# Performance work log

Hardware: AMD Instinct MI355X
Metric: run time of the kernel (lower is better)

## Reference

```python
import jax, jax.numpy as jnp
import numpy as np

B, N, H, D = 8, 2048, 4, 64  # batch, seq, heads (multi_head_count), head_dim
OUT = 256


def setup_inputs() -> dict:
    key = jax.random.key(0)
    ks = jax.random.split(key, 9)
    s = 0.02
    return {
        "x": jax.random.normal(ks[0], (B, N, H * D), dtype=jnp.float32),
        "Wq": jax.random.normal(ks[1], (H, D, D), dtype=jnp.float32) * s,
        "Wk": jax.random.normal(ks[2], (H, D, D), dtype=jnp.float32) * s,
        "Wv": jax.random.normal(ks[3], (H, D, D), dtype=jnp.float32) * s,
        "bq": jnp.zeros((H, D), dtype=jnp.float32),
        "bk": jnp.zeros((H, D), dtype=jnp.float32),
        "bv": jnp.zeros((H, D), dtype=jnp.float32),
        "Wp": jax.random.normal(ks[4], (H * D, OUT), dtype=jnp.float32) * s,
        "bp": jnp.zeros((OUT,), dtype=jnp.float32),
    }


def reference(x, Wq, Wk, Wv, bq, bk, bv, Wp, bp):
    # x: [b, n, h*d] -> [b, h, n, d]
    b, n, _ = x.shape
    xh = x.reshape(b, n, H, D).transpose(0, 2, 1, 3)
    # per-head Q/K/V with per-head weights (heads selected = [0..H-1], deterministic for num_heads==4)
    q = jnp.einsum("bhnd,hde->bhne", xh, Wq) + bq[None, :, None, :]
    k = jnp.einsum("bhnd,hde->bhne", xh, Wk) + bk[None, :, None, :]
    v = jnp.einsum("bhnd,hde->bhne", xh, Wv) + bv[None, :, None, :]
    scale = 1.0 / jnp.sqrt(jnp.asarray(D, dtype=x.dtype))
    scores = jnp.einsum("bhne,bhme->bhnm", q, k) * scale  # [b,h,n,n]
    attn = jax.nn.softmax(scores, axis=-1)
    o = jnp.einsum("bhnm,bhme->bhne", attn, v)  # [b,h,n,d]
    # concat heads: [b, n, h*d], then final projection
    o = o.transpose(0, 2, 1, 3).reshape(b, n, H * D)
    return o @ Wp + bp
```

## Files before the change

### kernel.cpp

```cpp
#include <hip/hip_runtime.h>

typedef __attribute__((ext_vector_type(4)))  float  f32x4;
typedef __attribute__((ext_vector_type(16))) float  f32x16;
typedef __attribute__((ext_vector_type(8)))  __bf16 bf16x8;
typedef __attribute__((ext_vector_type(2)))  unsigned u32x2;

constexpr int Bv = 8, Nv = 2048, Hv = 4, Dv = 64, OUTv = 256, HD = 256;
constexpr int BH = Bv * Hv;
constexpr size_t PH = (size_t)BH * Nv * Dv;

#if __has_builtin(__builtin_amdgcn_exp2f)
#define EXP2(x) __builtin_amdgcn_exp2f(x)
#else
#define EXP2(x) exp2f(x)
#endif

__device__ __forceinline__ unsigned short f2bf(float f) {
    union { __bf16 h; unsigned short u; } r;
    r.h = (__bf16)f;
    return r.u;
}

__device__ __forceinline__ unsigned pk_bf16(float a, float b) {
    union { __bf16 h[2]; unsigned u; } r;
    r.h[0] = (__bf16)a; r.h[1] = (__bf16)b;
    return r.u;
}

__device__ __forceinline__ uint4 pack8(const float* f) {
    uint4 u;
    u.x = pk_bf16(f[0], f[1]);
    u.y = pk_bf16(f[2], f[3]);
    u.z = pk_bf16(f[4], f[5]);
    u.w = pk_bf16(f[6], f[7]);
    return u;
}

__device__ __forceinline__ void swap32(unsigned a, unsigned b, unsigned& lo, unsigned& hi) {
#if __has_builtin(__builtin_amdgcn_permlane32_swap)
    u32x2 r = __builtin_amdgcn_permlane32_swap(a, b, false, false);
    lo = r.x; hi = r.y;
#else
    const int ishi = (threadIdx.x & 63) >> 5;
    unsigned pa = __shfl_xor(a, 32, 64), pb = __shfl_xor(b, 32, 64);
    lo = ishi ? pb : a;
    hi = ishi ? b : pa;
#endif
}

#define GLOBAL_AS __attribute__((address_space(1)))
#define LDS_AS    __attribute__((address_space(3)))

__global__ __launch_bounds__(256) void wconv_kernel(
    const float* __restrict__ Wq, const float* __restrict__ Wk, const float* __restrict__ Wv,
    const float* __restrict__ Wp,
    unsigned short* __restrict__ Wt3, unsigned short* __restrict__ Wpt)
{
    const int idx = blockIdx.x * 256 + threadIdx.x;
    if (idx < 49152) {
        const int m = idx >> 14, r = idx & 16383;
        const int h = r >> 12, e = (r >> 6) & 63, d = r & 63;
        const float* W = (m == 0) ? Wq : ((m == 1) ? Wk : Wv);
        Wt3[idx] = f2bf(W[(h << 12) + d * 64 + e]);
    } else {
        const int r = idx - 49152;
        const int e = r >> 8, c = r & 255;
        Wpt[r] = f2bf(Wp[c * 256 + e]);
    }
}

__global__ __launch_bounds__(256) void qkv_kernel(
    const float* __restrict__ x,
    const unsigned short* __restrict__ Wt3,
    const float* __restrict__ bq, const float* __restrict__ bk, const float* __restrict__ bv,
    unsigned short* __restrict__ Qb, unsigned short* __restrict__ Kb,
    unsigned short* __restrict__ Vt)
{
    const int h = blockIdx.x & 3;
    const int tt = blockIdx.x >> 2;
    const int tok0 = tt * 64;
    const int t = threadIdx.x, l = t & 63, w = t >> 6;
    const int lg = l >> 4, lc = l & 15;

    __shared__ uint4 Xs[64 * 8];
    __shared__ uint4 Ws[3 * 512];
    __shared__ uint4 Os[64 * 8];

#pragma unroll
    for (int k = 0; k < 6; ++k) {
        const int s = k * 256 + t;
        const int m = s >> 9, sm = s & 511;
        const int e = sm >> 3, cp = sm & 7;
        __builtin_amdgcn_global_load_lds(
            (const GLOBAL_AS unsigned int*)(Wt3 + (m << 14) + (h << 12) + (e << 6) + ((cp ^ (e & 7)) << 3)),
            (LDS_AS unsigned int*)((char*)Ws + (k * 256 + w * 64) * 16),
            16, 0, 0);
    }

    {
        const int r = t >> 2, c4 = t & 3;
        const float* src = x + (size_t)(tok0 + r) * HD + h * Dv + c4 * 16;
        float f[16];
        *(float4*)(f)      = *(const float4*)(src);
        *(float4*)(f + 4)  = *(const float4*)(src + 4);
        *(float4*)(f + 8)  = *(const float4*)(src + 8);
        *(float4*)(f + 12) = *(const float4*)(src + 12);
        Xs[r * 8 + ((c4 * 2)     ^ (r & 7))] = pack8(f);
        Xs[r * 8 + ((c4 * 2 + 1) ^ (r & 7))] = pack8(f + 8);
    }
    asm volatile("s_waitcnt vmcnt(0)" ::: "memory");
    __syncthreads();

    const int ar = w * 16 + lc;
    bf16x8 a[2];
    a[0] = ((const bf16x8*)Xs)[ar * 8 + (lg       ^ (ar & 7))];
    a[1] = ((const bf16x8*)Xs)[ar * 8 + ((4 + lg) ^ (ar & 7))];

    f32x4 acc[3][4];
#pragma unroll
    for (int m = 0; m < 3; ++m)
#pragma unroll
        for (int nt = 0; nt < 4; ++nt) acc[m][nt] = (f32x4){0.f, 0.f, 0.f, 0.f};

#pragma unroll
    for (int kk = 0; kk < 2; ++kk) {
#pragma unroll
        for (int m = 0; m < 3; ++m) {
#pragma unroll
            for (int nt = 0; nt < 4; ++nt) {
                const int br = nt * 16 + lc;
                const bf16x8 b = ((const bf16x8*)Ws)[(m << 9) + br * 8 + ((kk * 4 + lg) ^ (br & 7))];
                acc[m][nt] = __builtin_amdgcn_mfma_f32_16x16x32_bf16(a[kk], b, acc[m][nt], 0, 0, 0);
            }
        }
    }

    const int b_ = tok0 >> 11, n_ = tok0 & (Nv - 1);
    const int bh = b_ * Hv + h;
    unsigned short* Os16 = (unsigned short*)Os;
    const float* biases[3] = {bq + h * Dv, bk + h * Dv, bv + h * Dv};
    const float QSCALE = 0.125f * 1.44269504088896340736f;

#pragma unroll
    for (int m = 0; m < 3; ++m) {
        if (m) __syncthreads();
        if (m < 2) {
#pragma unroll
            for (int nt = 0; nt < 4; ++nt) {
                const int e = nt * 16 + lc;
                const float bias = biases[m][e];
#pragma unroll
                for (int j = 0; j < 4; ++j) {
                    float v = acc[m][nt][j] + bias;
                    if (m == 0) v *= QSCALE;
                    const int row = w * 16 + lg * 4 + j;
                    const int ch = (e >> 3) ^ (row & 7);
                    Os16[row * 64 + ch * 8 + (e & 7)] = f2bf(v);
                }
            }
            __syncthreads();
            const int r = t >> 2, c4 = t & 3;
            unsigned short* dst = (m == 0 ? Qb : Kb) + ((size_t)bh * Nv + n_ + r) * Dv + c4 * 16;
            *(uint4*)dst       = Os[r * 8 + ((c4 * 2)     ^ (r & 7))];
            *(uint4*)(dst + 8) = Os[r * 8 + ((c4 * 2 + 1) ^ (r & 7))];
        } else {
#pragma unroll
            for (int nt = 0; nt < 4; ++nt) {
                const int e = nt * 16 + lc;
                const float bias = biases[2][e];
#pragma unroll
                for (int j = 0; j < 4; ++j) {
                    const int tok = w * 16 + lg * 4 + j;
                    const int ch = (tok >> 3) ^ (e & 7);
                    Os16[e * 64 + ch * 8 + (tok & 7)] = f2bf(acc[2][nt][j] + bias);
                }
            }
            __syncthreads();
            const int e = t >> 2, c4 = t & 3;
            unsigned short* dst = Vt + ((size_t)bh * Dv + e) * Nv + n_ + c4 * 16;
            *(uint4*)dst       = Os[e * 8 + ((c4 * 2)     ^ (e & 7))];
            *(uint4*)(dst + 8) = Os[e * 8 + ((c4 * 2 + 1) ^ (e & 7))];
        }
    }
}

__global__ __launch_bounds__(256, 2) void attn_kernel(
    const unsigned short* __restrict__ Qb, const unsigned short* __restrict__ Kb,
    const unsigned short* __restrict__ Vt, unsigned short* __restrict__ Ob)
{
    const int bh = blockIdx.x & 31;
    const int qt = blockIdx.x >> 5;
    const int t = threadIdx.x, w = t >> 6, l = t & 63;
    const int hi = l >> 5, lc = l & 31;

    __shared__ uint4 Ks[2][128 * 8];
    __shared__ uint4 Vs[2][64 * 16];

    const unsigned short* Kg = Kb + (size_t)bh * Nv * Dv;
    const unsigned short* Vg = Vt + (size_t)bh * Dv * Nv;

    const int q_ = qt * 128 + w * 32 + lc;
    const unsigned short* Qrow = Qb + ((size_t)bh * Nv + q_) * Dv;
    bf16x8 qf[4];
#pragma unroll
    for (int kk = 0; kk < 4; ++kk)
        qf[kk] = *(const bf16x8*)(Qrow + kk * 16 + hi * 8);

    auto stage = [&](int buf, int kt) {
#pragma unroll
        for (int k = 0; k < 4; ++k) {
            const int s = k * 256 + t;
            const int base = k * 256 + w * 64;
            {
                const int r = s >> 3, c = (s & 7) ^ (r & 7);
                __builtin_amdgcn_global_load_lds(
                    (const GLOBAL_AS unsigned int*)(Kg + ((size_t)kt * 128 + r) * Dv + c * 8),
                    (LDS_AS unsigned int*)((char*)&Ks[buf][0] + base * 16),
                    16, 0, 0);
            }
            {
                const int r = s >> 4, c = (s & 15) ^ (r & 15);
                __builtin_amdgcn_global_load_lds(
                    (const GLOBAL_AS unsigned int*)(Vg + (size_t)r * Nv + kt * 128 + c * 8),
                    (LDS_AS unsigned int*)((char*)&Vs[buf][0] + base * 16),
                    16, 0, 0);
            }
        }
    };

    f32x16 o0, o1;
#pragma unroll
    for (int i = 0; i < 16; ++i) { o0[i] = 0.f; o1[i] = 0.f; }
    float m_run = -1e30f, l_part = 0.f;

    stage(0, 0);
    asm volatile("s_waitcnt vmcnt(0)" ::: "memory");
    __syncthreads();

    int cur = 0;
    for (int kt = 0; kt < Nv / 128; ++kt) {
        if (kt < Nv / 128 - 1) stage(cur ^ 1, kt + 1);

        const uint4* KsB = &Ks[cur][0];
        const uint4* VsB = &Vs[cur][0];

        f32x16 s4[4];
#pragma unroll
        for (int nt = 0; nt < 4; ++nt) {
#pragma unroll
            for (int i = 0; i < 16; ++i) s4[nt][i] = 0.f;
        }
        __builtin_amdgcn_s_setprio(1);
#pragma unroll
        for (int kk = 0; kk < 4; ++kk) {
#pragma unroll
            for (int nt = 0; nt < 4; ++nt) {
                const int r = nt * 32 + lc;
                const bf16x8 af = *(const bf16x8*)&KsB[r * 8 + ((kk * 2 + hi) ^ (r & 7))];
                s4[nt] = __builtin_amdgcn_mfma_f32_32x32x16_bf16(af, qf[kk], s4[nt], 0, 0, 0);
            }
        }
        __builtin_amdgcn_s_setprio(0);

        float v16[16];
#pragma unroll
        for (int r = 0; r < 16; ++r)
            v16[r] = fmaxf(fmaxf(s4[0][r], s4[1][r]), fmaxf(s4[2][r], s4[3][r]));
#pragma unroll
        for (int st = 8; st; st >>= 1)
#pragma unroll
            for (int r = 0; r < st; ++r) v16[r] = fmaxf(v16[r], v16[r + st]);
        float tm = fmaxf(v16[0], __shfl_xor(v16[0], 32, 64));

        if (!__all(tm <= m_run + 8.f)) {
            const float m_new = fmaxf(m_run, tm);
            const float sc = EXP2(m_run - m_new);
            m_run = m_new;
            l_part *= sc;
#pragma unroll
            for (int i = 0; i < 16; ++i) { o0[i] *= sc; o1[i] *= sc; }
        }

        float tsa[4] = {0.f, 0.f, 0.f, 0.f};
#pragma unroll
        for (int nt = 0; nt < 4; ++nt) {
#pragma unroll
            for (int r = 0; r < 16; ++r) {
                const float p = EXP2(s4[nt][r] - m_run);
                s4[nt][r] = p;
                tsa[r & 3] += p;
            }
            unsigned c[8];
#pragma unroll
            for (int i = 0; i < 8; ++i) c[i] = pk_bf16(s4[nt][2 * i], s4[nt][2 * i + 1]);

            unsigned d0a, d2a, d1a, d3a, d0b, d2b, d1b, d3b;
            swap32(c[0], c[2], d0a, d2a);
            swap32(c[1], c[3], d1a, d3a);
            swap32(c[4], c[6], d0b, d2b);
            swap32(c[5], c[7], d1b, d3b);

            union { unsigned u[4]; bf16x8 v; } pf0, pf1;
            pf0.u[0] = d0a; pf0.u[1] = d1a; pf0.u[2] = d2a; pf0.u[3] = d3a;
            pf1.u[0] = d0b; pf1.u[1] = d1b; pf1.u[2] = d2b; pf1.u[3] = d3b;

            __builtin_amdgcn_s_setprio(1);
#pragma unroll
            for (int kslow = 0; kslow < 2; ++kslow) {
                const bf16x8 pf = kslow ? pf1.v : pf0.v;
                {
                    const int row = lc;
                    const int ch = (nt * 4 + kslow * 2 + hi) ^ (row & 15);
                    const bf16x8 vf = *(const bf16x8*)&VsB[row * 16 + ch];
                    o0 = __builtin_amdgcn_mfma_f32_32x32x16_bf16(vf, pf, o0, 0, 0, 0);
                }
                {
                    const int row = 32 + lc;
                    const int ch = (nt * 4 + kslow * 2 + hi) ^ (row & 15);
                    const bf16x8 vf = *(const bf16x8*)&VsB[row * 16 + ch];
                    o1 = __builtin_amdgcn_mfma_f32_32x32x16_bf16(vf, pf, o1, 0, 0, 0);
                }
            }
            __builtin_amdgcn_s_setprio(0);
        }
        l_part += (tsa[0] + tsa[1]) + (tsa[2] + tsa[3]);

        if (kt < Nv / 128 - 1) {
            asm volatile("s_waitcnt vmcnt(0)" ::: "memory");
            __syncthreads();
            cur ^= 1;
        }
    }

    const float lf = l_part + __shfl_xor(l_part, 32, 64);
    const float inv = 1.0f / lf;
    const int b_ = bh >> 2, h_ = bh & 3;
    unsigned short* orow = Ob + ((size_t)b_ * Nv + q_) * HD + h_ * Dv;
#pragma unroll
    for (int g = 0; g < 4; ++g) {
        uint2 ua, ub;
        ua.x = pk_bf16(o0[g * 4 + 0] * inv, o0[g * 4 + 1] * inv);
        ua.y = pk_bf16(o0[g * 4 + 2] * inv, o0[g * 4 + 3] * inv);
        ub.x = pk_bf16(o1[g * 4 + 0] * inv, o1[g * 4 + 1] * inv);
        ub.y = pk_bf16(o1[g * 4 + 2] * inv, o1[g * 4 + 3] * inv);
        *(uint2*)(orow + 8 * g + 4 * hi)      = ua;
        *(uint2*)(orow + 32 + 8 * g + 4 * hi) = ub;
    }
}

__global__ __launch_bounds__(256) void proj_kernel(
    const unsigned short* __restrict__ Ob, const unsigned short* __restrict__ Wpt,
    const float* __restrict__ bp, float* __restrict__ out)
{
    const int tok0 = blockIdx.x * 64;
    const int t = threadIdx.x, w = t >> 6, l = t & 63;
    const int hi = l >> 5, lc = l & 31;
    const int tw = w >> 1;

    __shared__ uint4 SH[2560];

    f32x16 acc[4];
#pragma unroll
    for (int ct = 0; ct < 4; ++ct)
#pragma unroll
        for (int i = 0; i < 16; ++i) acc[ct][i] = 0.f;

    for (int kt = 0; kt < 4; ++kt) {
        const int c0 = kt * 64;
        if (kt) __syncthreads();
#pragma unroll
        for (int j = 0; j < 10; ++j) {
            const int s = j * 256 + t;
            const int base = j * 256 + w * 64;
            if (s < 512) {
                const int r = s >> 3, cp = s & 7;
                __builtin_amdgcn_global_load_lds(
                    (const GLOBAL_AS unsigned int*)(Ob + (size_t)(tok0 + r) * HD + c0 + ((cp ^ (r & 7)) << 3)),
                    (LDS_AS unsigned int*)((char*)SH + base * 16),
                    16, 0, 0);
            } else {
                const int sm = s - 512;
                const int e = sm >> 3, cp = sm & 7;
                __builtin_amdgcn_global_load_lds(
                    (const GLOBAL_AS unsigned int*)(Wpt + (size_t)e * HD + c0 + ((cp ^ (e & 7)) << 3)),
                    (LDS_AS unsigned int*)((char*)SH + base * 16),
                    16, 0, 0);
            }
        }
        asm volatile("s_waitcnt vmcnt(0)" ::: "memory");
        __syncthreads();

        const bf16x8* Osh = (const bf16x8*)SH;
        const bf16x8* Wsh = (const bf16x8*)(SH + 512);
        const int r = tw * 32 + lc;
#pragma unroll
        for (int kk = 0; kk < 4; ++kk) {
            const bf16x8 af = Osh[r * 8 + ((kk * 2 + hi) ^ (r & 7))];
#pragma unroll
            for (int ct = 0; ct < 4; ++ct) {
                const int e = (w & 1) * 128 + ct * 32 + lc;
                const bf16x8 bf = Wsh[e * 8 + ((kk * 2 + hi) ^ (e & 7))];
                acc[ct] = __builtin_amdgcn_mfma_f32_32x32x16_bf16(af, bf, acc[ct], 0, 0, 0);
            }
        }
    }

#pragma unroll
    for (int ct = 0; ct < 4; ++ct) {
        const int e = (w & 1) * 128 + ct * 32 + lc;
        const float bias = bp[e];
#pragma unroll
        for (int r = 0; r < 16; ++r) {
            const int tok = tok0 + tw * 32 + (r & 3) + 8 * (r >> 2) + 4 * hi;
            out[(size_t)tok * OUTv + e] = acc[ct][r] + bias;
        }
    }
}

extern "C" void kernel_launch(void* const* d_in, const int* in_sizes, int n_in,
                              void* d_out, int out_size, void* d_ws, size_t ws_size,
                              hipStream_t stream)
{
    const float* x  = (const float*)d_in[0];
    const float* Wq = (const float*)d_in[1];
    const float* Wk = (const float*)d_in[2];
    const float* Wv = (const float*)d_in[3];
    const float* bq = (const float*)d_in[4];
    const float* bk = (const float*)d_in[5];
    const float* bv = (const float*)d_in[6];
    const float* Wp = (const float*)d_in[7];
    const float* bp = (const float*)d_in[8];
    float* out = (float*)d_out;

    unsigned short* us = (unsigned short*)d_ws;
    unsigned short* Qb  = us;
    unsigned short* Kb  = us + PH;
    unsigned short* Vt  = us + 2 * PH;
    unsigned short* Ob  = us + 3 * PH;
    unsigned short* Wt3 = us + 4 * PH;
    unsigned short* Wpt = Wt3 + 49152;

    wconv_kernel<<<448, 256, 0, stream>>>(Wq, Wk, Wv, Wp, Wt3, Wpt);
    qkv_kernel<<<(Bv * Nv / 64) * Hv, 256, 0, stream>>>(x, Wt3, bq, bk, bv, Qb, Kb, Vt);
    attn_kernel<<<(Nv / 128) * BH, 256, 0, stream>>>(Qb, Kb, Vt, Ob);
    proj_kernel<<<Bv * Nv / 64, 256, 0, stream>>>(Ob, Wpt, bp, out);
}
```

Baseline: 154.6 us.

## Pre-convert x to bf16, merge QKV epilogue, double-buffer smaller proj tiles

x is converted to bf16 in the weight-conversion kernel, so the QKV kernel can load it straight into LDS with global_load_lds instead of doing fp32 loads and packing in registers. The QKV epilogue now writes Q, K and V^T into three LDS regions in one pass with two barriers instead of six. The projection kernel moves to 32-token tiles with double-buffered LDS staging, which overlaps loads with MFMA and doubles the grid. The cost is an extra bf16 round trip of x through global memory.

```diff
diff --git a/kernel.cpp b/kernel.cpp
--- a/kernel.cpp
+++ b/kernel.cpp
@@ -52,11 +52,21 @@
 #define LDS_AS    __attribute__((address_space(3)))
 
 __global__ __launch_bounds__(256) void wconv_kernel(
+    const float* __restrict__ x,
     const float* __restrict__ Wq, const float* __restrict__ Wk, const float* __restrict__ Wv,
     const float* __restrict__ Wp,
+    unsigned short* __restrict__ Xb,
     unsigned short* __restrict__ Wt3, unsigned short* __restrict__ Wpt)
 {
-    const int idx = blockIdx.x * 256 + threadIdx.x;
+    if (blockIdx.x < 2048) {
+        const size_t g = ((size_t)blockIdx.x * 256 + threadIdx.x) * 8;
+        float f[8];
+        *(float4*)(f)     = *(const float4*)(x + g);
+        *(float4*)(f + 4) = *(const float4*)(x + g + 4);
+        *(uint4*)(Xb + g) = pack8(f);
+        return;
+    }
+    const int idx = (blockIdx.x - 2048) * 256 + threadIdx.x;
     if (idx < 49152) {
         const int m = idx >> 14, r = idx & 16383;
         const int h = r >> 12, e = (r >> 6) & 63, d = r & 63;
@@ -70,7 +80,7 @@
 }
 
 __global__ __launch_bounds__(256) void qkv_kernel(
-    const float* __restrict__ x,
+    const unsigned short* __restrict__ Xb,
     const unsigned short* __restrict__ Wt3,
     const float* __restrict__ bq, const float* __restrict__ bk, const float* __restrict__ bv,
     unsigned short* __restrict__ Qb, unsigned short* __restrict__ Kb,
@@ -87,6 +97,16 @@
     __shared__ uint4 Os[64 * 8];
 
 #pragma unroll
+    for (int k = 0; k < 2; ++k) {
+        const int slot = k * 256 + t;
+        const int r = slot >> 3, cp = slot & 7;
+        const int c = cp ^ (r & 7);
+        __builtin_amdgcn_global_load_lds(
+            (const GLOBAL_AS unsigned int*)(Xb + (size_t)(tok0 + r) * HD + h * Dv + c * 8),
+            (LDS_AS unsigned int*)((char*)Xs + (k * 256 + w * 64) * 16),
+            16, 0, 0);
+    }
+#pragma unroll
     for (int k = 0; k < 6; ++k) {
         const int s = k * 256 + t;
         const int m = s >> 9, sm = s & 511;
@@ -96,18 +116,6 @@
             (LDS_AS unsigned int*)((char*)Ws + (k * 256 + w * 64) * 16),
             16, 0, 0);
     }
-
-    {
-        const int r = t >> 2, c4 = t & 3;
-        const float* src = x + (size_t)(tok0 + r) * HD + h * Dv + c4 * 16;
-        float f[16];
-        *(float4*)(f)      = *(const float4*)(src);
-        *(float4*)(f + 4)  = *(const float4*)(src + 4);
-        *(float4*)(f + 8)  = *(const float4*)(src + 8);
-        *(float4*)(f + 12) = *(const float4*)(src + 12);
-        Xs[r * 8 + ((c4 * 2)     ^ (r & 7))] = pack8(f);
-        Xs[r * 8 + ((c4 * 2 + 1) ^ (r & 7))] = pack8(f + 8);
-    }
     asm volatile("s_waitcnt vmcnt(0)" ::: "memory");
     __syncthreads();
 
@@ -137,50 +145,42 @@
 
     const int b_ = tok0 >> 11, n_ = tok0 & (Nv - 1);
     const int bh = b_ * Hv + h;
-    unsigned short* Os16 = (unsigned short*)Os;
-    const float* biases[3] = {bq + h * Dv, bk + h * Dv, bv + h * Dv};
     const float QSCALE = 0.125f * 1.44269504088896340736f;
 
-#pragma unroll
-    for (int m = 0; m < 3; ++m) {
-        if (m) __syncthreads();
-        if (m < 2) {
-#pragma unroll
-            for (int nt = 0; nt < 4; ++nt) {
-                const int e = nt * 16 + lc;
-                const float bias = biases[m][e];
-#pragma unroll
-                for (int j = 0; j < 4; ++j) {
-                    float v = acc[m][nt][j] + bias;
-                    if (m == 0) v *= QSCALE;
-                    const int row = w * 16 + lg * 4 + j;
-                    const int ch = (e >> 3) ^ (row & 7);
-                    Os16[row * 64 + ch * 8 + (e & 7)] = f2bf(v);
-                }
-            }
-            __syncthreads();
-            const int r = t >> 2, c4 = t & 3;
-            unsigned short* dst = (m == 0 ? Qb : Kb) + ((size_t)bh * Nv + n_ + r) * Dv + c4 * 16;
-            *(uint4*)dst       = Os[r * 8 + ((c4 * 2)     ^ (r & 7))];
-            *(uint4*)(dst + 8) = Os[r * 8 + ((c4 * 2 + 1) ^ (r & 7))];
-        } else {
-#pragma unroll
-            for (int nt = 0; nt < 4; ++nt) {
-                const int e = nt * 16 + lc;
-                const float bias = biases[2][e];
-#pragma unroll
-                for (int j = 0; j < 4; ++j) {
-                    const int tok = w * 16 + lg * 4 + j;
-                    const int ch = (tok >> 3) ^ (e & 7);
-                    Os16[e * 64 + ch * 8 + (tok & 7)] = f2bf(acc[2][nt][j] + bias);
-                }
-            }
-            __syncthreads();
-            const int e = t >> 2, c4 = t & 3;
-            unsigned short* dst = Vt + ((size_t)bh * Dv + e) * Nv + n_ + c4 * 16;
-            *(uint4*)dst       = Os[e * 8 + ((c4 * 2)     ^ (e & 7))];
-            *(uint4*)(dst + 8) = Os[e * 8 + ((c4 * 2 + 1) ^ (e & 7))];
-        }
+    __syncthreads();
+    {
+        unsigned short* Os16 = (unsigned short*)Os;
+        unsigned short* Ks16 = (unsigned short*)Xs;
+        unsigned short* Vs16 = (unsigned short*)Ws;
+#pragma unroll
+        for (int nt = 0; nt < 4; ++nt) {
+            const int e = nt * 16 + lc;
+            const float bq_ = bq[h * Dv + e];
+            const float bk_ = bk[h * Dv + e];
+            const float bv_ = bv[h * Dv + e];
+#pragma unroll
+            for (int j = 0; j < 4; ++j) {
+                const int row = w * 16 + lg * 4 + j;
+                const int ch = (e >> 3) ^ (row & 7);
+                Os16[row * 64 + ch * 8 + (e & 7)] = f2bf((acc[0][nt][j] + bq_) * QSCALE);
+                Ks16[row * 64 + ch * 8 + (e & 7)] = f2bf(acc[1][nt][j] + bk_);
+                const int chv = (row >> 3) ^ (e & 7);
+                Vs16[e * 64 + chv * 8 + (row & 7)] = f2bf(acc[2][nt][j] + bv_);
+            }
+        }
+    }
+    __syncthreads();
+    {
+        const int r = t >> 2, c4 = t & 3;
+        unsigned short* dq = Qb + ((size_t)bh * Nv + n_ + r) * Dv + c4 * 16;
+        *(uint4*)dq       = Os[r * 8 + ((c4 * 2)     ^ (r & 7))];
+        *(uint4*)(dq + 8) = Os[r * 8 + ((c4 * 2 + 1) ^ (r & 7))];
+        unsigned short* dk = Kb + ((size_t)bh * Nv + n_ + r) * Dv + c4 * 16;
+        *(uint4*)dk       = Xs[r * 8 + ((c4 * 2)     ^ (r & 7))];
+        *(uint4*)(dk + 8) = Xs[r * 8 + ((c4 * 2 + 1) ^ (r & 7))];
+        unsigned short* dv = Vt + ((size_t)bh * Dv + r) * Nv + n_ + c4 * 16;
+        *(uint4*)dv       = Ws[r * 8 + ((c4 * 2)     ^ (r & 7))];
+        *(uint4*)(dv + 8) = Ws[r * 8 + ((c4 * 2 + 1) ^ (r & 7))];
     }
 }
 
@@ -352,66 +352,73 @@
     const unsigned short* __restrict__ Ob, const unsigned short* __restrict__ Wpt,
     const float* __restrict__ bp, float* __restrict__ out)
 {
-    const int tok0 = blockIdx.x * 64;
+    const int tok0 = blockIdx.x * 32;
     const int t = threadIdx.x, w = t >> 6, l = t & 63;
     const int hi = l >> 5, lc = l & 31;
-    const int tw = w >> 1;
-
-    __shared__ uint4 SH[2560];
-
-    f32x16 acc[4];
-#pragma unroll
-    for (int ct = 0; ct < 4; ++ct)
-#pragma unroll
-        for (int i = 0; i < 16; ++i) acc[ct][i] = 0.f;
-
-    for (int kt = 0; kt < 4; ++kt) {
+
+    __shared__ uint4 SH[2][2304];
+
+    auto stage = [&](int buf, int kt) {
         const int c0 = kt * 64;
-        if (kt) __syncthreads();
-#pragma unroll
-        for (int j = 0; j < 10; ++j) {
+#pragma unroll
+        for (int j = 0; j < 9; ++j) {
             const int s = j * 256 + t;
             const int base = j * 256 + w * 64;
-            if (s < 512) {
+            if (s < 256) {
                 const int r = s >> 3, cp = s & 7;
                 __builtin_amdgcn_global_load_lds(
                     (const GLOBAL_AS unsigned int*)(Ob + (size_t)(tok0 + r) * HD + c0 + ((cp ^ (r & 7)) << 3)),
-                    (LDS_AS unsigned int*)((char*)SH + base * 16),
+                    (LDS_AS unsigned int*)((char*)&SH[buf][0] + base * 16),
                     16, 0, 0);
             } else {
-                const int sm = s - 512;
-                const int e = sm >> 3, cp = sm & 7;
+                const int s2 = s - 256;
+                const int e = s2 >> 3, cp = s2 & 7;
                 __builtin_amdgcn_global_load_lds(
                     (const GLOBAL_AS unsigned int*)(Wpt + (size_t)e * HD + c0 + ((cp ^ (e & 7)) << 3)),
-                    (LDS_AS unsigned int*)((char*)SH + base * 16),
+                    (LDS_AS unsigned int*)((char*)&SH[buf][0] + base * 16),
                     16, 0, 0);
             }
         }
-        asm volatile("s_waitcnt vmcnt(0)" ::: "memory");
+    };
+
+    f32x16 acc[2];
+#pragma unroll
+    for (int ct = 0; ct < 2; ++ct)
+#pragma unroll
+        for (int i = 0; i < 16; ++i) acc[ct][i] = 0.f;
+
+    stage(0, 0);
+    for (int kt = 0; kt < 4; ++kt) {
+        if (kt < 3) {
+            stage((kt + 1) & 1, kt + 1);
+            asm volatile("s_waitcnt vmcnt(9)" ::: "memory");
+        } else {
+            asm volatile("s_waitcnt vmcnt(0)" ::: "memory");
+        }
         __syncthreads();
 
-        const bf16x8* Osh = (const bf16x8*)SH;
-        const bf16x8* Wsh = (const bf16x8*)(SH + 512);
-        const int r = tw * 32 + lc;
+        const bf16x8* Osh = (const bf16x8*)&SH[kt & 1][0];
+        const bf16x8* Wsh = (const bf16x8*)&SH[kt & 1][256];
 #pragma unroll
         for (int kk = 0; kk < 4; ++kk) {
-            const bf16x8 af = Osh[r * 8 + ((kk * 2 + hi) ^ (r & 7))];
-#pragma unroll
-            for (int ct = 0; ct < 4; ++ct) {
-                const int e = (w & 1) * 128 + ct * 32 + lc;
-                const bf16x8 bf = Wsh[e * 8 + ((kk * 2 + hi) ^ (e & 7))];
-                acc[ct] = __builtin_amdgcn_mfma_f32_32x32x16_bf16(af, bf, acc[ct], 0, 0, 0);
-            }
-        }
-    }
-
-#pragma unroll
-    for (int ct = 0; ct < 4; ++ct) {
-        const int e = (w & 1) * 128 + ct * 32 + lc;
+            const bf16x8 af = Osh[lc * 8 + ((kk * 2 + hi) ^ (lc & 7))];
+#pragma unroll
+            for (int ct = 0; ct < 2; ++ct) {
+                const int e = w * 64 + ct * 32 + lc;
+                const bf16x8 bf_ = Wsh[e * 8 + ((kk * 2 + hi) ^ (e & 7))];
+                acc[ct] = __builtin_amdgcn_mfma_f32_32x32x16_bf16(af, bf_, acc[ct], 0, 0, 0);
+            }
+        }
+        __syncthreads();
+    }
+
+#pragma unroll
+    for (int ct = 0; ct < 2; ++ct) {
+        const int e = w * 64 + ct * 32 + lc;
         const float bias = bp[e];
 #pragma unroll
         for (int r = 0; r < 16; ++r) {
-            const int tok = tok0 + tw * 32 + (r & 3) + 8 * (r >> 2) + 4 * hi;
+            const int tok = tok0 + (r & 3) + 8 * (r >> 2) + 4 * hi;
             out[(size_t)tok * OUTv + e] = acc[ct][r] + bias;
         }
     }
@@ -437,11 +444,12 @@
     unsigned short* Kb  = us + PH;
     unsigned short* Vt  = us + 2 * PH;
     unsigned short* Ob  = us + 3 * PH;
-    unsigned short* Wt3 = us + 4 * PH;
+    unsigned short* Xb  = us + 4 * PH;
+    unsigned short* Wt3 = us + 5 * PH;
     unsigned short* Wpt = Wt3 + 49152;
 
-    wconv_kernel<<<448, 256, 0, stream>>>(Wq, Wk, Wv, Wp, Wt3, Wpt);
-    qkv_kernel<<<(Bv * Nv / 64) * Hv, 256, 0, stream>>>(x, Wt3, bq, bk, bv, Qb, Kb, Vt);
+    wconv_kernel<<<2048 + 448, 256, 0, stream>>>(x, Wq, Wk, Wv, Wp, Xb, Wt3, Wpt);
+    qkv_kernel<<<(Bv * Nv / 64) * Hv, 256, 0, stream>>>(Xb, Wt3, bq, bk, bv, Qb, Kb, Vt);
     attn_kernel<<<(Nv / 128) * BH, 256, 0, stream>>>(Qb, Kb, Vt, Ob);
-    proj_kernel<<<Bv * Nv / 64, 256, 0, stream>>>(Ob, Wpt, bp, out);
-}
+    proj_kernel<<<Bv * Nv / 32, 256, 0, stream>>>(Ob, Wpt, bp, out);
+}
```

Result: no change. 156.0 us (+0.9%).
